# Optimization experiments

Hardware: AMD Instinct MI355X
Metric: run time of the kernel (lower is better)

## Reference

```python
import jax, jax.numpy as jnp
import numpy as np

N_NODES = 100000
N_EDGES = 1600000
IN_C, HID_C, OUT_C = 64, 64, 40


def setup_inputs() -> dict:
    key = jax.random.key(0)
    ks = jax.random.split(key, 8)
    x = jax.random.normal(ks[0], (N_NODES, IN_C), dtype=jnp.float32)
    edge_index = jax.random.randint(ks[1], (2, N_EDGES), 0, N_NODES, dtype=jnp.int32)
    s = 1.0 / np.sqrt(HID_C)
    W1 = jax.random.uniform(ks[2], (IN_C, HID_C), jnp.float32, -s, s)
    b1 = jnp.zeros((HID_C,), jnp.float32)
    Wh = jax.random.uniform(ks[3], (HID_C, HID_C), jnp.float32, -s, s)
    bh = jnp.zeros((HID_C,), jnp.float32)
    W2 = jax.random.uniform(ks[4], (HID_C, OUT_C), jnp.float32, -s, s)
    b2 = jnp.zeros((OUT_C,), jnp.float32)
    return {"x": x, "edge_index": edge_index, "W1": W1, "b1": b1,
            "Wh": Wh, "bh": bh, "W2": W2, "b2": b2}


def reference(x, edge_index, W1, b1, Wh, bh, W2, b2):
    N = x.shape[0]
    loop = jnp.arange(N, dtype=edge_index.dtype)
    # GCN normalization with self-loops: A_hat = D^-1/2 (A + I) D^-1/2
    src = jnp.concatenate([edge_index[0], loop])  # [E + N]
    dst = jnp.concatenate([edge_index[1], loop])
    deg = jax.ops.segment_sum(jnp.ones_like(dst, dtype=x.dtype), dst, num_segments=N)
    dinv = jnp.where(deg > 0, jax.lax.rsqrt(deg), 0.0)
    norm = dinv[src] * dinv[dst]  # [E + N]

    def gcn_conv(h, W, b):
        h = h @ W                              # [N, out]
        msg = h[src] * norm[:, None]           # gather + scale, [E+N, out]
        return jax.ops.segment_sum(msg, dst, num_segments=N) + b

    h = jax.nn.relu(gcn_conv(x, W1, b1))       # conv1 (dropout = identity in eval)
    h = jax.nn.relu(gcn_conv(h, Wh, bh))       # hidden_conv, layer_size=2 -> one pass
    h = gcn_conv(h, W2, b2)                    # conv2
    return jax.nn.log_softmax(h, axis=1)
```

## Files before the change

kernel.cpp:

```cpp
#include <hip/hip_runtime.h>
#include <hip/hip_bf16.h>
#include <math.h>

#define EPT 16
#define BCAP 16384

typedef _Float16 half8 __attribute__((ext_vector_type(8)));
typedef _Float16 half2v __attribute__((ext_vector_type(2)));
typedef float f32x4 __attribute__((ext_vector_type(4)));

__device__ __forceinline__ unsigned short f16r(float f) {
    _Float16 h = (_Float16)f;
    return __builtin_bit_cast(unsigned short, h);
}
__device__ __forceinline__ half2v h2(unsigned u) {
    return __builtin_bit_cast(half2v, u);
}


__global__ void scat1_kernel(const int* __restrict__ src, const int* __restrict__ dst,
                             int* __restrict__ cntg, unsigned* __restrict__ ebuf, int E) {
    __shared__ int lh[256];
    __shared__ int lbase[256];
    int tid = threadIdx.x;
    lh[tid] = 0;
    __syncthreads();
    int base = blockIdx.x * (256 * EPT);
    int ds[EPT], ss[EPT];
#pragma unroll
    for (int k = 0; k < EPT; ++k) {
        int e = base + k * 256 + tid;
        ds[k] = (e < E) ? dst[e] : -1;
        ss[k] = (e < E) ? src[e] : 0;
    }
#pragma unroll
    for (int k = 0; k < EPT; ++k) {
        if (ds[k] >= 0) atomicAdd(&lh[ds[k] >> 9], 1);
    }
    __syncthreads();
    if (lh[tid] > 0) lbase[tid] = atomicAdd(&cntg[tid], lh[tid]);
    lh[tid] = 0;
    __syncthreads();
#pragma unroll
    for (int k = 0; k < EPT; ++k) {
        if (ds[k] >= 0) {
            int b = ds[k] >> 9;
            int pos = lbase[b] + atomicAdd(&lh[b], 1);
            ebuf[(size_t)b * BCAP + pos] = ((unsigned)ss[k] << 9) | (unsigned)(ds[k] & 511);
        }
    }
}

__global__ void build_kernel(const unsigned* __restrict__ ebuf, const int* __restrict__ cntg,
                             int* __restrict__ row_ptr, int* __restrict__ col,
                             float* __restrict__ dinv, int N, int E) {
    __shared__ int deg[512];
    __shared__ int sh[256];
    int b = blockIdx.x;
    int tid = threadIdx.x;

    int v = cntg[tid];
    sh[tid] = v;
    __syncthreads();
    int val = v;
    for (int off = 1; off < 256; off <<= 1) {
        int add = 0;
        if (tid >= off) add = sh[tid - off];
        __syncthreads();
        val += add;
        sh[tid] = val;
        __syncthreads();
    }
    int start = (b > 0) ? sh[b - 1] : 0;
    int cnt = cntg[b];
    __syncthreads();

    int nodeBase = b << 9;
    int nn = N - nodeBase;
    if (nn > 512) nn = 512;
    if (nn < 0) nn = 0;
    const unsigned* eb = ebuf + (size_t)b * BCAP;

    deg[tid] = 0;
    deg[tid + 256] = 0;
    __syncthreads();
    for (int j = tid; j < cnt; j += 256) {
        atomicAdd(&deg[eb[j] & 511u], 1);
    }
    __syncthreads();

    int i0 = tid * 2, i1 = i0 + 1;
    int v0 = deg[i0], v1 = deg[i1];
    int tot = v0 + v1;
    sh[tid] = tot;
    __syncthreads();
    int val2 = tot;
    for (int off = 1; off < 256; off <<= 1) {
        int add = 0;
        if (tid >= off) add = sh[tid - off];
        __syncthreads();
        val2 += add;
        sh[tid] = val2;
        __syncthreads();
    }
    int excl = val2 - tot;

    if (i0 < nn) { row_ptr[nodeBase + i0] = start + excl;      dinv[nodeBase + i0] = rsqrtf((float)v0 + 1.0f); }
    if (i1 < nn) { row_ptr[nodeBase + i1] = start + excl + v0; dinv[nodeBase + i1] = rsqrtf((float)v1 + 1.0f); }
    if (b == 0 && tid == 0) row_ptr[N] = E;
    deg[i0] = start + excl;
    deg[i1] = start + excl + v0;
    __syncthreads();

    for (int j = tid; j < cnt; j += 256) {
        unsigned rec = eb[j];
        int pos = atomicAdd(&deg[rec & 511u], 1);
        col[pos] = (int)(rec >> 9);
    }
}


__global__ void cvtpack_kernel(const float* __restrict__ x, unsigned short* __restrict__ xb,
                               int n4, int npad, const float* __restrict__ dinv,
                               const float* __restrict__ W1, const float* __restrict__ Wh,
                               const float* __restrict__ W2, unsigned short* __restrict__ wp1,
                               unsigned short* __restrict__ wph, unsigned short* __restrict__ wp2) {
    int bid = blockIdx.x;
    if (bid < 16) {
        int i = bid * 256 + threadIdx.x;
        int j = i & 7;
        int lane = (i >> 3) & 63;
        int hh = (i >> 9) & 1;
        int t = i >> 10;
        int k = hh * 32 + (lane >> 4) * 8 + j;
        int cc = t * 16 + (lane & 15);
        wp1[i] = f16r(W1[k * 64 + cc]);
        wph[i] = f16r(Wh[k * 64 + cc]);
        if (t < 3) wp2[i] = f16r(cc < 40 ? W2[k * 40 + cc] : 0.f);
    } else {
        if (bid == 16 && threadIdx.x < 8) {
            *(uint4*)(xb + (size_t)npad * 64 + threadIdx.x * 8) = make_uint4(0, 0, 0, 0);
        }
        int i = (bid - 16) * 256 + threadIdx.x;
        if (i < n4) {
            float dn = dinv[i >> 4];
            float4 v = *(const float4*)(x + (size_t)i * 4);
            ushort4 o;
            o.x = f16r(v.x * dn); o.y = f16r(v.y * dn);
            o.z = f16r(v.z * dn); o.w = f16r(v.w * dn);
            *(ushort4*)(xb + (size_t)i * 4) = o;
        }
    }
}


__launch_bounds__(256, 8)
__global__ void agg_kernel(const unsigned short* __restrict__ h, const int* __restrict__ row_ptr,
                           const int* __restrict__ col, const float* __restrict__ dinv,
                           unsigned short* __restrict__ aggout, int n, int zrow) {
    int tid = threadIdx.x;
    int lane = tid & 63;
    int node = blockIdx.x * 4 + (tid >> 6);
    if (node >= n) return;

    int sub = lane >> 3;
    unsigned choff = (lane & 7) * 16u;

    int beg = row_ptr[node];
    int deg = row_ptr[node + 1] - beg;
    float di = dinv[node];
    int total = deg + 1;

    half2v a0 = (half2v)0, a1 = (half2v)0, a2 = (half2v)0, a3 = (half2v)0;

    int base = 0;
    while (base < total) {
        int vi = base + lane;
        int idx = zrow;
        if (vi < deg) idx = col[beg + vi];
        else if (vi == deg) idx = node;
        int cnt = min(total - base, 64);
#pragma unroll
        for (int it = 0; it < 4; ++it) {
            int c0 = it * 16;
            if (c0 >= cnt) break;
            int s0 = __shfl(idx, c0 + sub);
            int s1 = __shfl(idx, c0 + 8 + sub);
            uint4 u0 = *(const uint4*)((const char*)h + (((unsigned)s0 << 7) + choff));
            uint4 u1 = *(const uint4*)((const char*)h + (((unsigned)s1 << 7) + choff));
            a0 += h2(u0.x);  a1 += h2(u0.y);  a2 += h2(u0.z);  a3 += h2(u0.w);
            a0 += h2(u1.x);  a1 += h2(u1.y);  a2 += h2(u1.z);  a3 += h2(u1.w);
        }
        base += cnt;
    }
#pragma unroll
    for (int off = 8; off <= 32; off <<= 1) {
        a0 += __builtin_bit_cast(half2v, __shfl_xor(__builtin_bit_cast(int, a0), off));
        a1 += __builtin_bit_cast(half2v, __shfl_xor(__builtin_bit_cast(int, a1), off));
        a2 += __builtin_bit_cast(half2v, __shfl_xor(__builtin_bit_cast(int, a2), off));
        a3 += __builtin_bit_cast(half2v, __shfl_xor(__builtin_bit_cast(int, a3), off));
    }

    if (sub == 0) {
        half2v dih = __builtin_bit_cast(half2v, __builtin_amdgcn_cvt_pkrtz(di, di));
        a0 *= dih; a1 *= dih; a2 *= dih; a3 *= dih;
        uint4 o;
        o.x = __builtin_bit_cast(unsigned, a0);
        o.y = __builtin_bit_cast(unsigned, a1);
        o.z = __builtin_bit_cast(unsigned, a2);
        o.w = __builtin_bit_cast(unsigned, a3);
        *(uint4*)((char*)aggout + (((unsigned)node << 7) + choff)) = o;
    }
}


__global__ void gemm_relu_kernel(const unsigned short* __restrict__ A,
                                 const unsigned short* __restrict__ wp,
                                 const float* __restrict__ bias,
                                 const float* __restrict__ dinv,
                                 unsigned short* __restrict__ out, int nTiles, int n, int zrow) {
    if (blockIdx.x == 0 && threadIdx.x < 8) {
        *(uint4*)(out + (size_t)zrow * 64 + threadIdx.x * 8) = make_uint4(0, 0, 0, 0);
    }
    int wv = blockIdx.x * 4 + (threadIdx.x >> 6);
    int lane = threadIdx.x & 63;
    if (wv >= nTiles) return;
    int q = lane >> 4, c = lane & 15;

    half8 bfrag[4][2];
#pragma unroll
    for (int t = 0; t < 4; ++t)
#pragma unroll
        for (int hh = 0; hh < 2; ++hh)
            bfrag[t][hh] = *(const half8*)(wp + t * 1024 + hh * 512 + lane * 8);
    float bs[4];
#pragma unroll
    for (int t = 0; t < 4; ++t) bs[t] = bias[t * 16 + c];

    int nodeBase = wv * 16;
    const unsigned short* arow = A + (size_t)(nodeBase + c) * 64 + q * 8;
    half8 a0 = *(const half8*)(arow);
    half8 a1 = *(const half8*)(arow + 32);

    f32x4 acc[4];
#pragma unroll
    for (int t = 0; t < 4; ++t) {
        f32x4 z = {0.f, 0.f, 0.f, 0.f};
        z = __builtin_amdgcn_mfma_f32_16x16x32_f16(a0, bfrag[t][0], z, 0, 0, 0);
        z = __builtin_amdgcn_mfma_f32_16x16x32_f16(a1, bfrag[t][1], z, 0, 0, 0);
        acc[t] = z;
    }

#pragma unroll
    for (int r = 0; r < 4; ++r) {
        int node = nodeBase + q * 4 + r;
        if (node < n) {
            float dn = dinv[node];
            unsigned short* orow = out + (size_t)node * 64;
#pragma unroll
            for (int t = 0; t < 4; ++t)
                orow[t * 16 + c] = f16r(fmaxf(acc[t][r] + bs[t], 0.f) * dn);
        }
    }
}

__global__ void gemm_lsm_kernel(const unsigned short* __restrict__ A,
                                const unsigned short* __restrict__ wp,
                                const float* __restrict__ bias,
                                float* __restrict__ out, int nTiles, int n) {
    int wv = blockIdx.x * 4 + (threadIdx.x >> 6);
    int lane = threadIdx.x & 63;
    if (wv >= nTiles) return;
    int q = lane >> 4, c = lane & 15;
    bool v2ok = (c < 8);

    half8 bfrag[3][2];
#pragma unroll
    for (int t = 0; t < 3; ++t)
#pragma unroll
        for (int hh = 0; hh < 2; ++hh)
            bfrag[t][hh] = *(const half8*)(wp + t * 1024 + hh * 512 + lane * 8);
    float bs[3];
    bs[0] = bias[c];
    bs[1] = bias[16 + c];
    bs[2] = v2ok ? bias[32 + c] : 0.f;

    int nodeBase = wv * 16;
    const unsigned short* arow = A + (size_t)(nodeBase + c) * 64 + q * 8;
    half8 a0 = *(const half8*)(arow);
    half8 a1 = *(const half8*)(arow + 32);

    f32x4 acc[3];
#pragma unroll
    for (int t = 0; t < 3; ++t) {
        f32x4 z = {0.f, 0.f, 0.f, 0.f};
        z = __builtin_amdgcn_mfma_f32_16x16x32_f16(a0, bfrag[t][0], z, 0, 0, 0);
        z = __builtin_amdgcn_mfma_f32_16x16x32_f16(a1, bfrag[t][1], z, 0, 0, 0);
        acc[t] = z;
    }

#pragma unroll
    for (int r = 0; r < 4; ++r) {
        int node = nodeBase + q * 4 + r;
        if (node < n) {
            float v0 = acc[0][r] + bs[0];
            float v1 = acc[1][r] + bs[1];
            float v2 = v2ok ? (acc[2][r] + bs[2]) : -INFINITY;
            float m = fmaxf(fmaxf(v0, v1), v2);
#pragma unroll
            for (int off = 1; off <= 8; off <<= 1) m = fmaxf(m, __shfl_xor(m, off));
            float s = expf(v0 - m) + expf(v1 - m) + (v2ok ? expf(v2 - m) : 0.f);
#pragma unroll
            for (int off = 1; off <= 8; off <<= 1) s += __shfl_xor(s, off);
            float ls = m + logf(s);
            float* orow = out + (size_t)node * 40;
            orow[c] = v0 - ls;
            orow[16 + c] = v1 - ls;
            if (v2ok) orow[32 + c] = v2 - ls;
        }
    }
}


extern "C" void kernel_launch(void* const* d_in, const int* in_sizes, int n_in,
                              void* d_out, int out_size, void* d_ws, size_t ws_size,
                              hipStream_t stream) {
    const float* x  = (const float*)d_in[0];
    const int* ei   = (const int*)d_in[1];
    const float* W1 = (const float*)d_in[2];
    const float* b1 = (const float*)d_in[3];
    const float* Wh = (const float*)d_in[4];
    const float* bh = (const float*)d_in[5];
    const float* W2 = (const float*)d_in[6];
    const float* b2 = (const float*)d_in[7];
    float* out = (float*)d_out;

    const int N = in_sizes[0] / 64;
    const int E = in_sizes[1] / 2;
    const int nbuk = (N + 511) >> 9;
    const int nTiles = (N + 15) / 16;
    const int Npad = nTiles * 16;

    const int* srcp = ei;
    const int* dstp = ei + E;

    size_t off = 0;
    auto alloc = [&](size_t bytes) {
        size_t o = off;
        off = (off + bytes + 255) & ~(size_t)255;
        return o;
    };
    char* ws = (char*)d_ws;
    int*      cntg    = (int*)(ws + alloc(256 * 4));
    int*      row_ptr = (int*)(ws + alloc((size_t)(N + 1) * 4));
    float*    dinv    = (float*)(ws + alloc((size_t)N * 4));
    int*      col     = (int*)(ws + alloc((size_t)E * 4));
    unsigned* ebuf    = (unsigned*)(ws + alloc((size_t)nbuk * BCAP * 4));
    unsigned short* wp1  = (unsigned short*)(ws + alloc(4096 * 2));
    unsigned short* wph  = (unsigned short*)(ws + alloc(4096 * 2));
    unsigned short* wp2  = (unsigned short*)(ws + alloc(3072 * 2));
    unsigned short* xb   = (unsigned short*)(ws + alloc((size_t)(Npad + 1) * 64 * 2));
    unsigned short* aggA = (unsigned short*)(ws + alloc((size_t)Npad * 64 * 2));
    unsigned short* gA   = (unsigned short*)(ws + alloc((size_t)(Npad + 1) * 64 * 2));
    (void)ws_size;

    hipMemsetAsync(cntg, 0, 256 * 4, stream);

    const int ebGrid = (E + 256 * EPT - 1) / (256 * EPT);
    scat1_kernel<<<ebGrid, 256, 0, stream>>>(srcp, dstp, cntg, ebuf, E);
    build_kernel<<<nbuk, 256, 0, stream>>>(ebuf, cntg, row_ptr, col, dinv, N, E);

    const int n4 = N * 16;
    cvtpack_kernel<<<16 + (n4 + 255) / 256, 256, 0, stream>>>(x, xb, n4, Npad, dinv,
                                                              W1, Wh, W2, wp1, wph, wp2);

    const int aggGrid = (N + 3) / 4;
    const int gemmGrid = (nTiles + 3) / 4;

    agg_kernel<<<aggGrid, 256, 0, stream>>>(xb, row_ptr, col, dinv, aggA, N, Npad);
    gemm_relu_kernel<<<gemmGrid, 256, 0, stream>>>(aggA, wp1, b1, dinv, gA, nTiles, N, Npad);
    agg_kernel<<<aggGrid, 256, 0, stream>>>(gA, row_ptr, col, dinv, aggA, N, Npad);
    gemm_relu_kernel<<<gemmGrid, 256, 0, stream>>>(aggA, wph, bh, dinv, gA, nTiles, N, Npad);
    agg_kernel<<<aggGrid, 256, 0, stream>>>(gA, row_ptr, col, dinv, aggA, N, Npad);
    gemm_lsm_kernel<<<gemmGrid, 256, 0, stream>>>(aggA, wp2, b2, out, nTiles, N);
}
```

Measured before the change: 267.1 us.

## Fuse weight packing into scatter and x conversion into CSR build; widen gather batch

Removes the separate cvtpack kernel. Weight packing now runs in extra leading blocks of the scatter kernel, and the dinv-scaled fp16 conversion of x runs per bucket inside build_kernel using dinv values held in shared memory. The aggregation loop also issues four gathers per step instead of two, giving more memory-level parallelism. The cost is one fewer launch and no global re-read of dinv, but build_kernel now carries more serial work per block across only about 196 blocks.

```diff
diff --git a/kernel.cpp b/kernel.cpp
--- a/kernel.cpp
+++ b/kernel.cpp
@@ -19,115 +19,12 @@
 
 
 __global__ void scat1_kernel(const int* __restrict__ src, const int* __restrict__ dst,
-                             int* __restrict__ cntg, unsigned* __restrict__ ebuf, int E) {
-    __shared__ int lh[256];
-    __shared__ int lbase[256];
-    int tid = threadIdx.x;
-    lh[tid] = 0;
-    __syncthreads();
-    int base = blockIdx.x * (256 * EPT);
-    int ds[EPT], ss[EPT];
-#pragma unroll
-    for (int k = 0; k < EPT; ++k) {
-        int e = base + k * 256 + tid;
-        ds[k] = (e < E) ? dst[e] : -1;
-        ss[k] = (e < E) ? src[e] : 0;
-    }
-#pragma unroll
-    for (int k = 0; k < EPT; ++k) {
-        if (ds[k] >= 0) atomicAdd(&lh[ds[k] >> 9], 1);
-    }
-    __syncthreads();
-    if (lh[tid] > 0) lbase[tid] = atomicAdd(&cntg[tid], lh[tid]);
-    lh[tid] = 0;
-    __syncthreads();
-#pragma unroll
-    for (int k = 0; k < EPT; ++k) {
-        if (ds[k] >= 0) {
-            int b = ds[k] >> 9;
-            int pos = lbase[b] + atomicAdd(&lh[b], 1);
-            ebuf[(size_t)b * BCAP + pos] = ((unsigned)ss[k] << 9) | (unsigned)(ds[k] & 511);
-        }
-    }
-}
-
-__global__ void build_kernel(const unsigned* __restrict__ ebuf, const int* __restrict__ cntg,
-                             int* __restrict__ row_ptr, int* __restrict__ col,
-                             float* __restrict__ dinv, int N, int E) {
-    __shared__ int deg[512];
-    __shared__ int sh[256];
-    int b = blockIdx.x;
-    int tid = threadIdx.x;
-
-    int v = cntg[tid];
-    sh[tid] = v;
-    __syncthreads();
-    int val = v;
-    for (int off = 1; off < 256; off <<= 1) {
-        int add = 0;
-        if (tid >= off) add = sh[tid - off];
-        __syncthreads();
-        val += add;
-        sh[tid] = val;
-        __syncthreads();
-    }
-    int start = (b > 0) ? sh[b - 1] : 0;
-    int cnt = cntg[b];
-    __syncthreads();
-
-    int nodeBase = b << 9;
-    int nn = N - nodeBase;
-    if (nn > 512) nn = 512;
-    if (nn < 0) nn = 0;
-    const unsigned* eb = ebuf + (size_t)b * BCAP;
-
-    deg[tid] = 0;
-    deg[tid + 256] = 0;
-    __syncthreads();
-    for (int j = tid; j < cnt; j += 256) {
-        atomicAdd(&deg[eb[j] & 511u], 1);
-    }
-    __syncthreads();
-
-    int i0 = tid * 2, i1 = i0 + 1;
-    int v0 = deg[i0], v1 = deg[i1];
-    int tot = v0 + v1;
-    sh[tid] = tot;
-    __syncthreads();
-    int val2 = tot;
-    for (int off = 1; off < 256; off <<= 1) {
-        int add = 0;
-        if (tid >= off) add = sh[tid - off];
-        __syncthreads();
-        val2 += add;
-        sh[tid] = val2;
-        __syncthreads();
-    }
-    int excl = val2 - tot;
-
-    if (i0 < nn) { row_ptr[nodeBase + i0] = start + excl;      dinv[nodeBase + i0] = rsqrtf((float)v0 + 1.0f); }
-    if (i1 < nn) { row_ptr[nodeBase + i1] = start + excl + v0; dinv[nodeBase + i1] = rsqrtf((float)v1 + 1.0f); }
-    if (b == 0 && tid == 0) row_ptr[N] = E;
-    deg[i0] = start + excl;
-    deg[i1] = start + excl + v0;
-    __syncthreads();
-
-    for (int j = tid; j < cnt; j += 256) {
-        unsigned rec = eb[j];
-        int pos = atomicAdd(&deg[rec & 511u], 1);
-        col[pos] = (int)(rec >> 9);
-    }
-}
-
-
-__global__ void cvtpack_kernel(const float* __restrict__ x, unsigned short* __restrict__ xb,
-                               int n4, int npad, const float* __restrict__ dinv,
-                               const float* __restrict__ W1, const float* __restrict__ Wh,
-                               const float* __restrict__ W2, unsigned short* __restrict__ wp1,
-                               unsigned short* __restrict__ wph, unsigned short* __restrict__ wp2) {
-    int bid = blockIdx.x;
-    if (bid < 16) {
-        int i = bid * 256 + threadIdx.x;
+                             int* __restrict__ cntg, unsigned* __restrict__ ebuf, int E,
+                             const float* __restrict__ W1, const float* __restrict__ Wh,
+                             const float* __restrict__ W2, unsigned short* __restrict__ wp1,
+                             unsigned short* __restrict__ wph, unsigned short* __restrict__ wp2) {
+    if (blockIdx.x < 16) {
+        int i = blockIdx.x * 256 + threadIdx.x;
         int j = i & 7;
         int lane = (i >> 3) & 63;
         int hh = (i >> 9) & 1;
@@ -137,19 +34,125 @@
         wp1[i] = f16r(W1[k * 64 + cc]);
         wph[i] = f16r(Wh[k * 64 + cc]);
         if (t < 3) wp2[i] = f16r(cc < 40 ? W2[k * 40 + cc] : 0.f);
-    } else {
-        if (bid == 16 && threadIdx.x < 8) {
-            *(uint4*)(xb + (size_t)npad * 64 + threadIdx.x * 8) = make_uint4(0, 0, 0, 0);
+        return;
+    }
+    __shared__ int lh[256];
+    __shared__ int lbase[256];
+    int tid = threadIdx.x;
+    lh[tid] = 0;
+    __syncthreads();
+    int base = (blockIdx.x - 16) * (256 * EPT);
+    int ds[EPT], ss[EPT];
+#pragma unroll
+    for (int k = 0; k < EPT; ++k) {
+        int e = base + k * 256 + tid;
+        ds[k] = (e < E) ? dst[e] : -1;
+        ss[k] = (e < E) ? src[e] : 0;
+    }
+#pragma unroll
+    for (int k = 0; k < EPT; ++k) {
+        if (ds[k] >= 0) atomicAdd(&lh[ds[k] >> 9], 1);
+    }
+    __syncthreads();
+    if (lh[tid] > 0) lbase[tid] = atomicAdd(&cntg[tid], lh[tid]);
+    lh[tid] = 0;
+    __syncthreads();
+#pragma unroll
+    for (int k = 0; k < EPT; ++k) {
+        if (ds[k] >= 0) {
+            int b = ds[k] >> 9;
+            int pos = lbase[b] + atomicAdd(&lh[b], 1);
+            ebuf[(size_t)b * BCAP + pos] = ((unsigned)ss[k] << 9) | (unsigned)(ds[k] & 511);
         }
-        int i = (bid - 16) * 256 + threadIdx.x;
-        if (i < n4) {
-            float dn = dinv[i >> 4];
-            float4 v = *(const float4*)(x + (size_t)i * 4);
-            ushort4 o;
-            o.x = f16r(v.x * dn); o.y = f16r(v.y * dn);
-            o.z = f16r(v.z * dn); o.w = f16r(v.w * dn);
-            *(ushort4*)(xb + (size_t)i * 4) = o;
-        }
+    }
+}
+
+
+__global__ void build_kernel(const unsigned* __restrict__ ebuf, const int* __restrict__ cntg,
+                             int* __restrict__ row_ptr, int* __restrict__ col,
+                             float* __restrict__ dinv, const float* __restrict__ x,
+                             unsigned short* __restrict__ xb, int N, int E, int npadRow) {
+    __shared__ int deg[512];
+    __shared__ int sh[256];
+    __shared__ float shd[512];
+    int b = blockIdx.x;
+    int tid = threadIdx.x;
+
+    int v = cntg[tid];
+    sh[tid] = v;
+    __syncthreads();
+    int val = v;
+    for (int off = 1; off < 256; off <<= 1) {
+        int add = 0;
+        if (tid >= off) add = sh[tid - off];
+        __syncthreads();
+        val += add;
+        sh[tid] = val;
+        __syncthreads();
+    }
+    int start = (b > 0) ? sh[b - 1] : 0;
+    int cnt = cntg[b];
+    __syncthreads();
+
+    int nodeBase = b << 9;
+    int nn = N - nodeBase;
+    if (nn > 512) nn = 512;
+    if (nn < 0) nn = 0;
+    const unsigned* eb = ebuf + (size_t)b * BCAP;
+
+    deg[tid] = 0;
+    deg[tid + 256] = 0;
+    __syncthreads();
+    for (int j = tid; j < cnt; j += 256) {
+        atomicAdd(&deg[eb[j] & 511u], 1);
+    }
+    __syncthreads();
+
+    int i0 = tid * 2, i1 = i0 + 1;
+    int v0 = deg[i0], v1 = deg[i1];
+    int tot = v0 + v1;
+    sh[tid] = tot;
+    __syncthreads();
+    int val2 = tot;
+    for (int off = 1; off < 256; off <<= 1) {
+        int add = 0;
+        if (tid >= off) add = sh[tid - off];
+        __syncthreads();
+        val2 += add;
+        sh[tid] = val2;
+        __syncthreads();
+    }
+    int excl = val2 - tot;
+
+    float d0 = rsqrtf((float)v0 + 1.0f);
+    float d1 = rsqrtf((float)v1 + 1.0f);
+    shd[i0] = d0;
+    shd[i1] = d1;
+    if (i0 < nn) { row_ptr[nodeBase + i0] = start + excl;      dinv[nodeBase + i0] = d0; }
+    if (i1 < nn) { row_ptr[nodeBase + i1] = start + excl + v0; dinv[nodeBase + i1] = d1; }
+    if (b == 0 && tid == 0) row_ptr[N] = E;
+    deg[i0] = start + excl;
+    deg[i1] = start + excl + v0;
+    __syncthreads();
+
+    for (int j = tid; j < cnt; j += 256) {
+        unsigned rec = eb[j];
+        int pos = atomicAdd(&deg[rec & 511u], 1);
+        col[pos] = (int)(rec >> 9);
+    }
+
+    int n4 = nn * 16;
+    for (int j = tid; j < n4; j += 256) {
+        int r = j >> 4;
+        float dn = shd[r];
+        float4 vx = ((const float4*)x)[(size_t)(nodeBase + r) * 16 + (j & 15)];
+        ushort4 o;
+        o.x = f16r(vx.x * dn); o.y = f16r(vx.y * dn);
+        o.z = f16r(vx.z * dn); o.w = f16r(vx.w * dn);
+        *(ushort4*)(xb + (size_t)(nodeBase + r) * 64 + (j & 15) * 4) = o;
+    }
+    if (b == 0 && tid < 8) {
+        *(uint4*)(xb + (size_t)npadRow * 64 + tid * 8) = make_uint4(0, 0, 0, 0);
     }
 }
 
@@ -181,15 +184,21 @@
         else if (vi == deg) idx = node;
         int cnt = min(total - base, 64);
 #pragma unroll
-        for (int it = 0; it < 4; ++it) {
-            int c0 = it * 16;
+        for (int half = 0; half < 2; ++half) {
+            int c0 = half * 32;
             if (c0 >= cnt) break;
             int s0 = __shfl(idx, c0 + sub);
             int s1 = __shfl(idx, c0 + 8 + sub);
+            int s2 = __shfl(idx, c0 + 16 + sub);
+            int s3 = __shfl(idx, c0 + 24 + sub);
             uint4 u0 = *(const uint4*)((const char*)h + (((unsigned)s0 << 7) + choff));
             uint4 u1 = *(const uint4*)((const char*)h + (((unsigned)s1 << 7) + choff));
+            uint4 u2 = *(const uint4*)((const char*)h + (((unsigned)s2 << 7) + choff));
+            uint4 u3 = *(const uint4*)((const char*)h + (((unsigned)s3 << 7) + choff));
             a0 += h2(u0.x);  a1 += h2(u0.y);  a2 += h2(u0.z);  a3 += h2(u0.w);
             a0 += h2(u1.x);  a1 += h2(u1.y);  a2 += h2(u1.z);  a3 += h2(u1.w);
+            a0 += h2(u2.x);  a1 += h2(u2.y);  a2 += h2(u2.z);  a3 += h2(u2.w);
+            a0 += h2(u3.x);  a1 += h2(u3.y);  a2 += h2(u3.z);  a3 += h2(u3.w);
         }
         base += cnt;
     }
@@ -367,12 +376,9 @@
     hipMemsetAsync(cntg, 0, 256 * 4, stream);
 
     const int ebGrid = (E + 256 * EPT - 1) / (256 * EPT);
-    scat1_kernel<<<ebGrid, 256, 0, stream>>>(srcp, dstp, cntg, ebuf, E);
-    build_kernel<<<nbuk, 256, 0, stream>>>(ebuf, cntg, row_ptr, col, dinv, N, E);
-
-    const int n4 = N * 16;
-    cvtpack_kernel<<<16 + (n4 + 255) / 256, 256, 0, stream>>>(x, xb, n4, Npad, dinv,
-                                                              W1, Wh, W2, wp1, wph, wp2);
+    scat1_kernel<<<16 + ebGrid, 256, 0, stream>>>(srcp, dstp, cntg, ebuf, E,
+                                                  W1, Wh, W2, wp1, wph, wp2);
+    build_kernel<<<nbuk, 256, 0, stream>>>(ebuf, cntg, row_ptr, col, dinv, x, xb, N, E, Npad);
 
     const int aggGrid = (N + 3) / 4;
     const int gemmGrid = (nTiles + 3) / 4;
```

After: 272.6 us. 2.0% more time.
